# Kernel tuning notes

Hardware: AMD Instinct MI355X
Metric: run time of the kernel (lower is better)

## Reference

```python
import math
import jax, jax.numpy as jnp
import numpy as np

N_HEADS = 16
D_EMBED = 1024

def setup_inputs() -> dict:
    key = jax.random.key(0)
    ks = jax.random.split(key, 5)
    b, l, d = 2, 2048, D_EMBED
    return {
        "x": jax.random.normal(ks[0], (b, l, d), dtype=jnp.float32),
        "w_in": jax.random.normal(ks[1], (3 * d, d), dtype=jnp.float32) * 0.02,
        "b_in": jax.random.normal(ks[2], (3 * d,), dtype=jnp.float32) * 0.02,
        "w_out": jax.random.normal(ks[3], (d, d), dtype=jnp.float32) * 0.02,
        "b_out": jax.random.normal(ks[4], (d,), dtype=jnp.float32) * 0.02,
    }

def reference(x, w_in, b_in, w_out, b_out):
    b, l, d = x.shape
    h = N_HEADS
    scale = 1.0 / math.sqrt(d // h)
    # in_proj then reshape to heads BEFORE chunking (faithful to source:
    # each head's 3*d_head block is split into q/k/v)
    x_proj = (x @ w_in.T + b_in).reshape(b, l, h, -1)  # (b,l,h,3*dh)
    q, k, v = jnp.split(x_proj, 3, axis=-1)            # each (b,l,h,dh)
    att = jnp.einsum('blhd,bmhd->blmh', q, k) * scale  # (b,l,m,h)
    # causal_mask=False path of the original forward
    att = jax.nn.softmax(att, axis=2)                  # softmax over keys m
    # faithful to source einsum 'blmh, blhd-> blhd' (sums att over m against
    # v indexed by l, exactly as the original code computes)
    opt = jnp.einsum('blmh,blhd->blhd', att, v).reshape(b, l, d)
    return opt @ w_out.T + b_out
```

## Files before the change

kernel.cpp:

```cpp
#include <hip/hip_runtime.h>

typedef unsigned short ushort_t;
typedef __bf16 bf16x8 __attribute__((ext_vector_type(8)));
typedef float f32x4 __attribute__((ext_vector_type(4)));

static __device__ __forceinline__ ushort_t f2bf(float f) {
    __bf16 b = (__bf16)f;
    return __builtin_bit_cast(ushort_t, b);
}

#define GLOAD_LDS16(gptr, lptr)                                                        \
    __builtin_amdgcn_global_load_lds(                                                  \
        (const __attribute__((address_space(1))) void*)(gptr),                         \
        (__attribute__((address_space(3))) void*)(lptr), 16, 0, 0)

#define CFENCE() asm volatile("" ::: "memory")

template <int N> __device__ __forceinline__ void waitcnt_vm() {
    if constexpr (N == 0) asm volatile("s_waitcnt vmcnt(0)" ::: "memory");
    else if constexpr (N == 2) asm volatile("s_waitcnt vmcnt(2)" ::: "memory");
    else if constexpr (N == 3) asm volatile("s_waitcnt vmcnt(3)" ::: "memory");
}

template <int BM, int BN, bool BF16_OUT>
__device__ __forceinline__
void gemm_core(const ushort_t* __restrict__ A, const ushort_t* __restrict__ B,
               const float* __restrict__ bias, void* __restrict__ C,
               const int K, const int N, const int rA, const int rB,
               ushort_t* ls) {
    constexpr int WM = BM / 2, WN = BN / 2;
    constexpr int MI = WM / 16, NJ = WN / 16;
    constexpr int LA = (BM * 32) / (8 * 256);
    constexpr int LB = (BN * 32) / (8 * 256);
    constexpr int HALF = (BM + BN) * 32;

    const int tid  = threadIdx.x;
    const int lane = tid & 63;
    const int wv   = tid >> 6;
    const int wr   = wv >> 1, wc = wv & 1;
    const int fr   = lane & 15, fq = lane >> 4;

    f32x4 acc[MI][NJ] = {};

    auto stage = [&](int k0, int buf) {
        #pragma unroll
        for (int q = 0; q < LA; ++q) {
            int c = q * 256 + tid;
            GLOAD_LDS16(A + (size_t)(rA + (c >> 2)) * K + k0 + (c & 3) * 8,
                        &ls[buf * HALF + c * 8]);
        }
        #pragma unroll
        for (int q = 0; q < LB; ++q) {
            int c = q * 256 + tid;
            GLOAD_LDS16(B + (size_t)(rB + (c >> 2)) * K + k0 + (c & 3) * 8,
                        &ls[buf * HALF + BM * 32 + c * 8]);
        }
    };

    const int T = K >> 5;
    stage(0, 0);
    for (int t = 0; t < T; ++t) {
        const int cur = t & 1;
        if (t + 1 < T) {
            stage((t + 1) << 5, cur ^ 1);
            waitcnt_vm<LA + LB>();
        } else {
            waitcnt_vm<0>();
        }
        __builtin_amdgcn_s_barrier();
        CFENCE();

        bf16x8 af[MI], bfv[NJ];
        #pragma unroll
        for (int i = 0; i < MI; ++i)
            af[i] = *(const bf16x8*)&ls[cur * HALF + (wr * WM + i * 16 + fr) * 32 + fq * 8];
        #pragma unroll
        for (int j = 0; j < NJ; ++j)
            bfv[j] = *(const bf16x8*)&ls[cur * HALF + BM * 32 + (wc * WN + j * 16 + fr) * 32 + fq * 8];
        #pragma unroll
        for (int i = 0; i < MI; ++i)
            #pragma unroll
            for (int j = 0; j < NJ; ++j)
                acc[i][j] = __builtin_amdgcn_mfma_f32_16x16x32_bf16(af[i], bfv[j], acc[i][j], 0, 0, 0);

        CFENCE();
        __builtin_amdgcn_s_barrier();
        CFENCE();
    }

    const int orow0 = rA + wr * WM + fq * 4;
    const int ocol0 = rB + wc * WN + fr;
    #pragma unroll
    for (int i = 0; i < MI; ++i)
        #pragma unroll
        for (int j = 0; j < NJ; ++j) {
            const int col = ocol0 + j * 16;
            const float bv = bias ? bias[col] : 0.f;
            #pragma unroll
            for (int r = 0; r < 4; ++r) {
                const int row = orow0 + i * 16 + r;
                const float v = acc[i][j][r] + bv;
                if constexpr (BF16_OUT)
                    ((ushort_t*)C)[(size_t)row * N + col] = f2bf(v);
                else
                    ((float*)C)[(size_t)row * N + col] = v;
            }
        }
}

__global__ __launch_bounds__(256)
void prep(const float* __restrict__ w_in, const float* __restrict__ b_in,
          const float* __restrict__ w_out, const float* __restrict__ b_out,
          ushort_t* __restrict__ wob, ushort_t* __restrict__ Pt,
          float* __restrict__ bfused) {
    __shared__ ushort_t tile[64][65];
    const int b = blockIdx.x;
    const int t = threadIdx.x;

    if (b < 128) {
        #pragma unroll
        for (int p = 0; p < 8; ++p) {
            int i = b * 2048 + p * 256 + t;
            float4 v = ((const float4*)w_out)[i];
            ushort4 o; o.x = f2bf(v.x); o.y = f2bf(v.y); o.z = f2bf(v.z); o.w = f2bf(v.w);
            ((ushort4*)wob)[i] = o;
        }
    } else if (b < 384) {
        const int g = b - 128;
        const int gx = g & 15, gy = g >> 4;
        #pragma unroll
        for (int p = 0; p < 16; ++p) {
            int e = p * 256 + t;
            int j = e >> 6, c = e & 63;
            tile[j][c] = f2bf(w_in[(size_t)(gx * 192 + 128 + j) * 1024 + gy * 64 + c]);
        }
        __syncthreads();
        #pragma unroll
        for (int p = 0; p < 16; ++p) {
            int e = p * 256 + t;
            int c = e >> 6, j = e & 63;
            Pt[(size_t)(gy * 64 + c) * 1024 + gx * 64 + j] = tile[j][c];
        }
    } else {
        const int w = t >> 6, lane = t & 63;
        const int row = (b - 384) * 4 + w;
        float s = 0.f;
        #pragma unroll
        for (int it = 0; it < 16; ++it) {
            int j = it * 64 + lane;
            int r = (j >> 6) * 192 + 128 + (j & 63);
            s += w_out[(size_t)row * 1024 + j] * b_in[r];
        }
        #pragma unroll
        for (int off = 32; off; off >>= 1) s += __shfl_down(s, off, 64);
        if (lane == 0) bfused[row] = s + b_out[row];
    }
}

__global__ __launch_bounds__(256)
void k2(const ushort_t* __restrict__ wob, const ushort_t* __restrict__ Pt,
        ushort_t* __restrict__ Wfb,
        const float* __restrict__ x, ushort_t* __restrict__ xb) {
    __shared__ alignas(16) ushort_t ls[(64 + 64) * 32 * 2];
    const int b = blockIdx.x;
    if (b < 256) {
        const int swz = (b & 7) * 32 + (b >> 3);
        const int by = swz >> 4, bx = swz & 15;
        gemm_core<64, 64, true>(wob, Pt, nullptr, (void*)Wfb, 1024, 1024,
                                by * 64, bx * 64, ls);
    } else {
        const int g = b - 256;
        const int t = threadIdx.x;
        #pragma unroll
        for (int p = 0; p < 8; ++p) {
            int i = g * 2048 + p * 256 + t;
            float4 v = ((const float4*)x)[i];
            ushort4 o; o.x = f2bf(v.x); o.y = f2bf(v.y); o.z = f2bf(v.z); o.w = f2bf(v.w);
            ((ushort4*)xb)[i] = o;
        }
    }
}

__global__ __launch_bounds__(256)
void k3(const ushort_t* __restrict__ xb, const ushort_t* __restrict__ Wfb,
        const float* __restrict__ bfused, float* __restrict__ out) {
    __shared__ alignas(16) ushort_t ls[(128 + 64) * 32 * 2];
    const int b = blockIdx.x;
    const int swz = (b & 7) * 64 + (b >> 3);
    const int by = swz >> 4, bx = swz & 15;
    gemm_core<128, 64, false>(xb, Wfb, bfused, (void*)out, 1024, 1024,
                              by * 128, bx * 64, ls);
}

extern "C" void kernel_launch(void* const* d_in, const int* in_sizes, int n_in,
                              void* d_out, int out_size, void* d_ws, size_t ws_size,
                              hipStream_t stream) {
    const float* x     = (const float*)d_in[0];
    const float* w_in  = (const float*)d_in[1];
    const float* b_in  = (const float*)d_in[2];
    const float* w_out = (const float*)d_in[3];
    const float* b_out = (const float*)d_in[4];
    float* out = (float*)d_out;

    char* ws = (char*)d_ws;
    ushort_t* xb     = (ushort_t*)(ws);
    ushort_t* wob    = (ushort_t*)(ws + (8u  << 20));
    ushort_t* Pt     = (ushort_t*)(ws + (10u << 20));
    ushort_t* Wfb    = (ushort_t*)(ws + (12u << 20));
    float*    bfused = (float*)   (ws + (14u << 20));

    prep<<<640, 256, 0, stream>>>(w_in, b_in, w_out, b_out, wob, Pt, bfused);
    k2<<<768, 256, 0, stream>>>(wob, Pt, Wfb, x, xb);
    k3<<<512, 256, 0, stream>>>(xb, Wfb, bfused, out);
}
```

Measured before the change: 40.21 us.

## Use triple-buffered LDS pipeline and 128x128 tiles for the final GEMM

The GEMM core moves from a double-buffered LDS pipeline to a three-stage one that keeps two tiles of global loads in flight, so load latency is hidden better. The main output GEMM (4096x1024x1024) switches from 128x64 tiles to 128x128 tiles. The grid drops from 512 to 256 blocks, which raises data reuse per block. In exchange, LDS use goes up, which can lower occupancy, and 256 blocks roughly match the CU count, so any tail imbalance costs more.

```diff
diff --git a/kernel.cpp b/kernel.cpp
--- a/kernel.cpp
+++ b/kernel.cpp
@@ -17,27 +17,29 @@
 #define CFENCE() asm volatile("" ::: "memory")
 
 template <int N> __device__ __forceinline__ void waitcnt_vm() {
-    if constexpr (N == 0) asm volatile("s_waitcnt vmcnt(0)" ::: "memory");
+    if constexpr (N == 0)      asm volatile("s_waitcnt vmcnt(0)" ::: "memory");
     else if constexpr (N == 2) asm volatile("s_waitcnt vmcnt(2)" ::: "memory");
-    else if constexpr (N == 3) asm volatile("s_waitcnt vmcnt(3)" ::: "memory");
-}
-
-template <int BM, int BN, bool BF16_OUT>
+    else if constexpr (N == 4) asm volatile("s_waitcnt vmcnt(4)" ::: "memory");
+    else if constexpr (N == 8) asm volatile("s_waitcnt vmcnt(8)" ::: "memory");
+}
+
+template <int BM, int BN, int WGM, int WGN, bool BF16_OUT>
 __device__ __forceinline__
 void gemm_core(const ushort_t* __restrict__ A, const ushort_t* __restrict__ B,
                const float* __restrict__ bias, void* __restrict__ C,
                const int K, const int N, const int rA, const int rB,
                ushort_t* ls) {
-    constexpr int WM = BM / 2, WN = BN / 2;
+    constexpr int WM = BM / WGM, WN = BN / WGN;
     constexpr int MI = WM / 16, NJ = WN / 16;
     constexpr int LA = (BM * 32) / (8 * 256);
     constexpr int LB = (BN * 32) / (8 * 256);
+    constexpr int L  = LA + LB;
     constexpr int HALF = (BM + BN) * 32;
 
     const int tid  = threadIdx.x;
     const int lane = tid & 63;
     const int wv   = tid >> 6;
-    const int wr   = wv >> 1, wc = wv & 1;
+    const int wr   = wv / WGN, wc = wv % WGN;
     const int fr   = lane & 15, fq = lane >> 4;
 
     f32x4 acc[MI][NJ] = {};
@@ -57,36 +59,42 @@
         }
     };
 
-    const int T = K >> 5;
-    stage(0, 0);
-    for (int t = 0; t < T; ++t) {
-        const int cur = t & 1;
-        if (t + 1 < T) {
-            stage((t + 1) << 5, cur ^ 1);
-            waitcnt_vm<LA + LB>();
-        } else {
-            waitcnt_vm<0>();
-        }
-        __builtin_amdgcn_s_barrier();
-        CFENCE();
-
+    auto compute = [&](int buf) {
         bf16x8 af[MI], bfv[NJ];
         #pragma unroll
         for (int i = 0; i < MI; ++i)
-            af[i] = *(const bf16x8*)&ls[cur * HALF + (wr * WM + i * 16 + fr) * 32 + fq * 8];
+            af[i] = *(const bf16x8*)&ls[buf * HALF + (wr * WM + i * 16 + fr) * 32 + fq * 8];
         #pragma unroll
         for (int j = 0; j < NJ; ++j)
-            bfv[j] = *(const bf16x8*)&ls[cur * HALF + BM * 32 + (wc * WN + j * 16 + fr) * 32 + fq * 8];
+            bfv[j] = *(const bf16x8*)&ls[buf * HALF + BM * 32 + (wc * WN + j * 16 + fr) * 32 + fq * 8];
         #pragma unroll
         for (int i = 0; i < MI; ++i)
             #pragma unroll
             for (int j = 0; j < NJ; ++j)
                 acc[i][j] = __builtin_amdgcn_mfma_f32_16x16x32_bf16(af[i], bfv[j], acc[i][j], 0, 0, 0);
-
-        CFENCE();
-        __builtin_amdgcn_s_barrier();
-        CFENCE();
+    };
+
+    const int T = K >> 5;
+    stage(0, 0);
+    stage(32, 1);
+    int cur = 0, nxt2 = 2;
+    for (int t = 0; t < T - 2; ++t) {
+        stage((t + 2) << 5, nxt2);
+        waitcnt_vm<2 * L>();
+        __builtin_amdgcn_s_barrier(); CFENCE();
+        compute(cur);
+        CFENCE(); __builtin_amdgcn_s_barrier(); CFENCE();
+        cur  = (cur  + 1 == 3) ? 0 : cur  + 1;
+        nxt2 = (nxt2 + 1 == 3) ? 0 : nxt2 + 1;
     }
+    waitcnt_vm<L>();
+    __builtin_amdgcn_s_barrier(); CFENCE();
+    compute(cur);
+    cur = (cur + 1 == 3) ? 0 : cur + 1;
+    CFENCE();
+    waitcnt_vm<0>();
+    __builtin_amdgcn_s_barrier(); CFENCE();
+    compute(cur);
 
     const int orow0 = rA + wr * WM + fq * 4;
     const int ocol0 = rB + wc * WN + fr;
@@ -161,13 +169,13 @@
 void k2(const ushort_t* __restrict__ wob, const ushort_t* __restrict__ Pt,
         ushort_t* __restrict__ Wfb,
         const float* __restrict__ x, ushort_t* __restrict__ xb) {
-    __shared__ alignas(16) ushort_t ls[(64 + 64) * 32 * 2];
+    __shared__ alignas(16) ushort_t ls[3 * (64 + 64) * 32];
     const int b = blockIdx.x;
     if (b < 256) {
         const int swz = (b & 7) * 32 + (b >> 3);
         const int by = swz >> 4, bx = swz & 15;
-        gemm_core<64, 64, true>(wob, Pt, nullptr, (void*)Wfb, 1024, 1024,
-                                by * 64, bx * 64, ls);
+        gemm_core<64, 64, 2, 2, true>(wob, Pt, nullptr, (void*)Wfb, 1024, 1024,
+                                      by * 64, bx * 64, ls);
     } else {
         const int g = b - 256;
         const int t = threadIdx.x;
@@ -184,12 +192,12 @@
 __global__ __launch_bounds__(256)
 void k3(const ushort_t* __restrict__ xb, const ushort_t* __restrict__ Wfb,
         const float* __restrict__ bfused, float* __restrict__ out) {
-    __shared__ alignas(16) ushort_t ls[(128 + 64) * 32 * 2];
+    __shared__ alignas(16) ushort_t ls[3 * (128 + 128) * 32];
     const int b = blockIdx.x;
-    const int swz = (b & 7) * 64 + (b >> 3);
-    const int by = swz >> 4, bx = swz & 15;
-    gemm_core<128, 64, false>(xb, Wfb, bfused, (void*)out, 1024, 1024,
-                              by * 128, bx * 64, ls);
+    const int swz = (b & 7) * 32 + (b >> 3);
+    const int by = swz >> 3, bx = swz & 7;
+    gemm_core<128, 128, 2, 2, false>(xb, Wfb, bfused, (void*)out, 1024, 1024,
+                                     by * 128, bx * 128, ls);
 }
 
 extern "C" void kernel_launch(void* const* d_in, const int* in_sizes, int n_in,
@@ -211,5 +219,5 @@
 
     prep<<<640, 256, 0, stream>>>(w_in, b_in, w_out, b_out, wob, Pt, bfused);
     k2<<<768, 256, 0, stream>>>(wob, Pt, Wfb, x, xb);
-    k3<<<512, 256, 0, stream>>>(xb, Wfb, bfused, out);
-}
+    k3<<<256, 256, 0, stream>>>(xb, Wfb, bfused, out);
+}
```

Result: faster. 37.23 us (-7.4%).
